# Optimization experiments

Measured on AMD Instinct MI355X. Metric: run time of the kernel, lower is better.

Reference implementation:

```python
import jax, jax.numpy as jnp
import numpy as np

B, I, O, G = 4096, 256, 256, 16


def setup_inputs() -> dict:
    key = jax.random.key(0)
    k1, k2 = jax.random.split(key)
    x = jax.random.normal(k1, (B, I), dtype=jnp.float32)
    # xavier_uniform bound for fan_in=I*G (last dim), fan_out=O treated per torch default on 4D: use small scale
    bound = float(np.sqrt(6.0 / (I * G + O * G)))
    laplacecoeffs = jax.random.uniform(k2, (2, O, I, G), dtype=jnp.float32, minval=-bound, maxval=bound)
    bias = jnp.zeros((1, O), dtype=jnp.float32)
    return {"x": x, "laplacecoeffs": laplacecoeffs, "bias": bias}


def reference(x, laplacecoeffs, bias):
    # x: (B, I); laplacecoeffs: (2, O, I, G); bias: (1, O)
    g = laplacecoeffs.shape[-1]  # static gridsize (clamped/rounded gridsize_param at init)
    lambdas = jnp.linspace(0.1, 1.0, g).astype(x.dtype)  # (G,)
    e = x[:, :, None] * lambdas  # (B, I, G)
    exp_neg = jnp.exp(-e)
    exp_pos = jnp.exp(e)
    # contract over (inputdim, gridsize) without materializing (B, O, I, G)
    y = jnp.einsum('big,oig->bo', exp_neg, laplacecoeffs[0])
    y = y + jnp.einsum('big,oig->bo', exp_pos, laplacecoeffs[1])
    y = y + bias  # (B, O)
    return y
```

## Files before the change

kernel.cpp:

```cpp
#include <hip/hip_runtime.h>


typedef __bf16 bf16x8 __attribute__((ext_vector_type(8)));
typedef __bf16 bf16x4 __attribute__((ext_vector_type(4)));
typedef float  f32x4  __attribute__((ext_vector_type(4)));

#define M_TOT 4096
#define N_TOT 256
#define MN_TOT (M_TOT * N_TOT)
#define SPLITK 8

__device__ __forceinline__ void gload_lds16(const __bf16* g, __bf16* l) {
  __builtin_amdgcn_global_load_lds(
      (const __attribute__((address_space(1))) void*)g,
      (__attribute__((address_space(3))) void*)l, 16, 0, 0);
}

__global__ void convert_w(const float* __restrict__ C, __bf16* __restrict__ W) {
  int t = blockIdx.x * 256 + threadIdx.x;
  int E = t << 2;
  int c = E >> 12, x4 = E & 4095;
  int s = c >> 8, o = c & 255;
  const f32x4 v = *(const f32x4*)(C + (size_t)c * 4096 + x4);
  bf16x4 w;
  w[0] = (__bf16)v[0]; w[1] = (__bf16)v[1]; w[2] = (__bf16)v[2]; w[3] = (__bf16)v[3];
  *(bf16x4*)(W + (size_t)o * 8192 + (size_t)s * 4096 + x4) = w;
}

template <int MODE>
__global__ __launch_bounds__(256, 2)
void laplace_gemm(const float* __restrict__ X, const __bf16* __restrict__ Wb,
                  const float* __restrict__ Bias, float* __restrict__ Out,
                  float* __restrict__ P) {
  __shared__ __bf16 As[128 * 72];
  __shared__ __bf16 Bs[128 * 64];

  const int tid = threadIdx.x;
  const int mt = blockIdx.x, nt = blockIdx.y, kt = blockIdx.z;
  const int m0 = mt * 128, n0 = nt * 128;
  const int s   = kt >> 2;
  const int i0c = (kt & 3) * 64;

  const int wv = tid >> 6, lane = tid & 63;
  const int wm = wv & 1, wn = wv >> 1;
  const int lm = lane & 15, q = lane >> 4;

  const int mr0 = tid >> 2,         ii0 = tid & 3;
  const int mr1 = (256 + tid) >> 2, ii1 = tid & 3;
  const float* xp0 = X + (size_t)(m0 + mr0) * 256 + i0c + ii0;
  const float* xp1 = X + (size_t)(m0 + mr1) * 256 + i0c + ii1;

  const float sgn = s ? 1.0f : -1.0f;
  const float c0 = 0.1f * sgn, cd = 0.06f * sgn;

  const f32x4 zero = {0.f, 0.f, 0.f, 0.f};
  f32x4 acc[4][4];
#pragma unroll
  for (int a = 0; a < 4; ++a)
#pragma unroll
    for (int b = 0; b < 4; ++b) acc[a][b] = zero;

  const size_t wrow = (size_t)s * 4096 + (size_t)i0c * 16;

  float xc0 = *xp0, xc1 = *xp1;

  for (int j = 0; j < 16; ++j) {
    const size_t kw = wrow + (size_t)j * 64;
#pragma unroll
    for (int qq = 0; qq < 4; ++qq) {
      const int idx = qq * 256 + tid;
      const int r = idx >> 3, cc = idx & 7;
      const __bf16* gsrc = Wb + (size_t)(n0 + r) * 8192 + kw + ((cc ^ (r & 7)) << 3);
      __bf16* ldst = Bs + ((qq * 256 + (tid & ~63)) << 3);
      gload_lds16(gsrc, ldst);
    }

    float xn0 = 0.f, xn1 = 0.f;
    if (j < 15) { xn0 = xp0[4 * (j + 1)]; xn1 = xp1[4 * (j + 1)]; }

    {
      const float p0 = __expf(c0 * xc0), rr = __expf(cd * xc0);
      bf16x8 v0, v1; float f = p0;
#pragma unroll
      for (int h = 0; h < 8; ++h) { v0[h] = (__bf16)f; f *= rr; }
#pragma unroll
      for (int h = 0; h < 8; ++h) { v1[h] = (__bf16)f; f *= rr; }
      *(bf16x8*)&As[mr0 * 72 + ii0 * 16]     = v0;
      *(bf16x8*)&As[mr0 * 72 + ii0 * 16 + 8] = v1;
    }
    {
      const float p0 = __expf(c0 * xc1), rr = __expf(cd * xc1);
      bf16x8 v0, v1; float f = p0;
#pragma unroll
      for (int h = 0; h < 8; ++h) { v0[h] = (__bf16)f; f *= rr; }
#pragma unroll
      for (int h = 0; h < 8; ++h) { v1[h] = (__bf16)f; f *= rr; }
      *(bf16x8*)&As[mr1 * 72 + ii1 * 16]     = v0;
      *(bf16x8*)&As[mr1 * 72 + ii1 * 16 + 8] = v1;
    }

    __syncthreads();

#pragma unroll
    for (int kk = 0; kk < 2; ++kk) {
      bf16x8 af[4], bf[4];
#pragma unroll
      for (int a = 0; a < 4; ++a)
        af[a] = *(const bf16x8*)&As[(wm * 64 + a * 16 + lm) * 72 + kk * 32 + q * 8];
      const int pc8 = (((kk << 2) + q) ^ (lm & 7)) << 3;
#pragma unroll
      for (int b = 0; b < 4; ++b)
        bf[b] = *(const bf16x8*)&Bs[(wn * 64 + b * 16 + lm) * 64 + pc8];
#pragma unroll
      for (int a = 0; a < 4; ++a)
#pragma unroll
        for (int b = 0; b < 4; ++b)
          acc[a][b] = __builtin_amdgcn_mfma_f32_16x16x32_bf16(af[a], bf[b], acc[a][b], 0, 0, 0);
    }
    __syncthreads();

    xc0 = xn0; xc1 = xn1;
  }

  if constexpr (MODE == 0) {
    float* Pk = P + (size_t)kt * MN_TOT;
#pragma unroll
    for (int a = 0; a < 4; ++a) {
      const int mrow = m0 + wm * 64 + a * 16 + q * 4;
#pragma unroll
      for (int rr = 0; rr < 4; ++rr)
#pragma unroll
        for (int b = 0; b < 4; ++b) {
          const int n = n0 + wn * 64 + b * 16 + lm;
          Pk[(size_t)(mrow + rr) * 256 + n] = acc[a][b][rr];
        }
    }
  } else {
#pragma unroll
    for (int a = 0; a < 4; ++a) {
      const int mrow = m0 + wm * 64 + a * 16 + q * 4;
#pragma unroll
      for (int rr = 0; rr < 4; ++rr)
#pragma unroll
        for (int b = 0; b < 4; ++b) {
          const int n = n0 + wn * 64 + b * 16 + lm;
          float v = acc[a][b][rr];
          if (kt == 0) v += Bias[n];
          atomicAdd(&Out[(size_t)(mrow + rr) * 256 + n], v);
        }
    }
  }
}

__global__ void reduce_bias(const float* __restrict__ P, const float* __restrict__ Bias,
                            float* __restrict__ Out) {
  const int t = blockIdx.x * 256 + threadIdx.x;
  const size_t base = (size_t)t * 4;
  f32x4 sv = *(const f32x4*)&P[base];
#pragma unroll
  for (int k = 1; k < SPLITK; ++k) sv += *(const f32x4*)&P[(size_t)k * MN_TOT + base];
  sv += *(const f32x4*)&Bias[base & 255];
  *(f32x4*)&Out[base] = sv;
}

extern "C" void kernel_launch(void* const* d_in, const int* in_sizes, int n_in,
                              void* d_out, int out_size, void* d_ws, size_t ws_size,
                              hipStream_t stream) {
  const float* X    = (const float*)d_in[0];
  const float* C    = (const float*)d_in[1];
  const float* Bias = (const float*)d_in[2];
  float* Out = (float*)d_out;

  __bf16* Wb = (__bf16*)d_ws;
  const size_t wb_bytes = (size_t)N_TOT * 8192 * sizeof(__bf16);
  const size_t p_bytes  = (size_t)SPLITK * MN_TOT * sizeof(float);
  float* P = (float*)((char*)d_ws + wb_bytes);

  convert_w<<<2048, 256, 0, stream>>>(C, Wb);

  if (ws_size >= wb_bytes + p_bytes) {
    laplace_gemm<0><<<dim3(32, 2, SPLITK), 256, 0, stream>>>(X, Wb, Bias, Out, P);
    reduce_bias<<<1024, 256, 0, stream>>>(P, Bias, Out);
  } else {
    hipMemsetAsync(d_out, 0, (size_t)out_size * sizeof(float), stream);
    laplace_gemm<1><<<dim3(32, 2, SPLITK), 256, 0, stream>>>(X, Wb, Bias, Out, P);
  }
}
```

Measured before the change: 93.33 us.

## Halve GEMM M-tile to 64 rows with 2-wave blocks and split exp recurrence

The GEMM block tile shrinks from 128x128 with 4 waves to 64x128 with 2 waves, doubling the grid to 1024 blocks so more CUs are busy. The serial 16-step multiply chain used to build the exponential grid values is split into two independent 8-step chains by precomputing r^8. Smaller tiles mean each B tile is reloaded from global memory twice as often, and fewer waves per block may hide latency less well.

```diff
diff --git a/kernel.cpp b/kernel.cpp
--- a/kernel.cpp
+++ b/kernel.cpp
@@ -28,25 +28,25 @@
 }
 
 template <int MODE>
-__global__ __launch_bounds__(256, 2)
+__global__ __launch_bounds__(128, 2)
 void laplace_gemm(const float* __restrict__ X, const __bf16* __restrict__ Wb,
                   const float* __restrict__ Bias, float* __restrict__ Out,
                   float* __restrict__ P) {
-  __shared__ __bf16 As[128 * 72];
+  __shared__ __bf16 As[64 * 72];
   __shared__ __bf16 Bs[128 * 64];
 
   const int tid = threadIdx.x;
   const int mt = blockIdx.x, nt = blockIdx.y, kt = blockIdx.z;
-  const int m0 = mt * 128, n0 = nt * 128;
+  const int m0 = mt * 64, n0 = nt * 128;
   const int s   = kt >> 2;
   const int i0c = (kt & 3) * 64;
 
   const int wv = tid >> 6, lane = tid & 63;
-  const int wm = wv & 1, wn = wv >> 1;
+  const int wn = wv;
   const int lm = lane & 15, q = lane >> 4;
 
   const int mr0 = tid >> 2,         ii0 = tid & 3;
-  const int mr1 = (256 + tid) >> 2, ii1 = tid & 3;
+  const int mr1 = (128 + tid) >> 2, ii1 = tid & 3;
   const float* xp0 = X + (size_t)(m0 + mr0) * 256 + i0c + ii0;
   const float* xp1 = X + (size_t)(m0 + mr1) * 256 + i0c + ii1;
 
@@ -67,11 +67,11 @@
   for (int j = 0; j < 16; ++j) {
     const size_t kw = wrow + (size_t)j * 64;
 #pragma unroll
-    for (int qq = 0; qq < 4; ++qq) {
-      const int idx = qq * 256 + tid;
+    for (int qq = 0; qq < 8; ++qq) {
+      const int idx = qq * 128 + tid;
       const int r = idx >> 3, cc = idx & 7;
       const __bf16* gsrc = Wb + (size_t)(n0 + r) * 8192 + kw + ((cc ^ (r & 7)) << 3);
-      __bf16* ldst = Bs + ((qq * 256 + (tid & ~63)) << 3);
+      __bf16* ldst = Bs + ((qq * 128 + (tid & ~63)) << 3);
       gload_lds16(gsrc, ldst);
     }
 
@@ -79,22 +79,24 @@
     if (j < 15) { xn0 = xp0[4 * (j + 1)]; xn1 = xp1[4 * (j + 1)]; }
 
     {
-      const float p0 = __expf(c0 * xc0), rr = __expf(cd * xc0);
-      bf16x8 v0, v1; float f = p0;
+      const float p = __expf(c0 * xc0), r = __expf(cd * xc0);
+      const float r2 = r * r, r4 = r2 * r2, r8 = r4 * r4;
+      bf16x8 v0, v1; float f = p, f2 = p * r8;
 #pragma unroll
-      for (int h = 0; h < 8; ++h) { v0[h] = (__bf16)f; f *= rr; }
+      for (int h = 0; h < 8; ++h) { v0[h] = (__bf16)f;  f  *= r; }
 #pragma unroll
-      for (int h = 0; h < 8; ++h) { v1[h] = (__bf16)f; f *= rr; }
+      for (int h = 0; h < 8; ++h) { v1[h] = (__bf16)f2; f2 *= r; }
       *(bf16x8*)&As[mr0 * 72 + ii0 * 16]     = v0;
       *(bf16x8*)&As[mr0 * 72 + ii0 * 16 + 8] = v1;
     }
     {
-      const float p0 = __expf(c0 * xc1), rr = __expf(cd * xc1);
-      bf16x8 v0, v1; float f = p0;
+      const float p = __expf(c0 * xc1), r = __expf(cd * xc1);
+      const float r2 = r * r, r4 = r2 * r2, r8 = r4 * r4;
+      bf16x8 v0, v1; float f = p, f2 = p * r8;
 #pragma unroll
-      for (int h = 0; h < 8; ++h) { v0[h] = (__bf16)f; f *= rr; }
+      for (int h = 0; h < 8; ++h) { v0[h] = (__bf16)f;  f  *= r; }
 #pragma unroll
-      for (int h = 0; h < 8; ++h) { v1[h] = (__bf16)f; f *= rr; }
+      for (int h = 0; h < 8; ++h) { v1[h] = (__bf16)f2; f2 *= r; }
       *(bf16x8*)&As[mr1 * 72 + ii1 * 16]     = v0;
       *(bf16x8*)&As[mr1 * 72 + ii1 * 16 + 8] = v1;
     }
@@ -103,19 +105,19 @@
 
 #pragma unroll
     for (int kk = 0; kk < 2; ++kk) {
-      bf16x8 af[4], bf[4];
+      bf16x8 af[4], bfr[4];
 #pragma unroll
       for (int a = 0; a < 4; ++a)
-        af[a] = *(const bf16x8*)&As[(wm * 64 + a * 16 + lm) * 72 + kk * 32 + q * 8];
+        af[a] = *(const bf16x8*)&As[(a * 16 + lm) * 72 + kk * 32 + q * 8];
       const int pc8 = (((kk << 2) + q) ^ (lm & 7)) << 3;
 #pragma unroll
       for (int b = 0; b < 4; ++b)
-        bf[b] = *(const bf16x8*)&Bs[(wn * 64 + b * 16 + lm) * 64 + pc8];
+        bfr[b] = *(const bf16x8*)&Bs[(wn * 64 + b * 16 + lm) * 64 + pc8];
 #pragma unroll
       for (int a = 0; a < 4; ++a)
 #pragma unroll
         for (int b = 0; b < 4; ++b)
-          acc[a][b] = __builtin_amdgcn_mfma_f32_16x16x32_bf16(af[a], bf[b], acc[a][b], 0, 0, 0);
+          acc[a][b] = __builtin_amdgcn_mfma_f32_16x16x32_bf16(af[a], bfr[b], acc[a][b], 0, 0, 0);
     }
     __syncthreads();
 
@@ -126,7 +128,7 @@
     float* Pk = P + (size_t)kt * MN_TOT;
 #pragma unroll
     for (int a = 0; a < 4; ++a) {
-      const int mrow = m0 + wm * 64 + a * 16 + q * 4;
+      const int mrow = m0 + a * 16 + q * 4;
 #pragma unroll
       for (int rr = 0; rr < 4; ++rr)
 #pragma unroll
@@ -138,7 +140,7 @@
   } else {
 #pragma unroll
     for (int a = 0; a < 4; ++a) {
-      const int mrow = m0 + wm * 64 + a * 16 + q * 4;
+      const int mrow = m0 + a * 16 + q * 4;
 #pragma unroll
       for (int rr = 0; rr < 4; ++rr)
 #pragma unroll
@@ -179,10 +181,10 @@
   convert_w<<<2048, 256, 0, stream>>>(C, Wb);
 
   if (ws_size >= wb_bytes + p_bytes) {
-    laplace_gemm<0><<<dim3(32, 2, SPLITK), 256, 0, stream>>>(X, Wb, Bias, Out, P);
+    laplace_gemm<0><<<dim3(64, 2, SPLITK), 128, 0, stream>>>(X, Wb, Bias, Out, P);
     reduce_bias<<<1024, 256, 0, stream>>>(P, Bias, Out);
   } else {
     hipMemsetAsync(d_out, 0, (size_t)out_size * sizeof(float), stream);
-    laplace_gemm<1><<<dim3(32, 2, SPLITK), 256, 0, stream>>>(X, Wb, Bias, Out, P);
+    laplace_gemm<1><<<dim3(64, 2, SPLITK), 128, 0, stream>>>(X, Wb, Bias, Out, P);
   }
 }
```

Result: no change. 94.67 us (+1.4%).
